# Kernel tuning notes

Measured on AMD Instinct MI355X. Metric: run time of the kernel, lower is better.

The kernel has to match this reference:

```python
import jax, jax.numpy as jnp
import numpy as np

N = 50000
E = 800000
G = 64  # number of graphs in each batch
IN_DIM = 128
HID = 64
NEG_SLOPE = 0.2


def _glorot(key, shape):
    fan = shape[0] + shape[-1] if len(shape) == 2 else int(np.prod(shape[1:])) + shape[-1]
    lim = float(np.sqrt(6.0 / fan))
    return jax.random.uniform(key, shape, jnp.float32, -lim, lim)


def setup_inputs() -> dict:
    key = jax.random.key(0)
    ks = jax.random.split(key, 16)
    x1 = jax.random.normal(ks[0], (N, IN_DIM), jnp.float32)
    x2 = jax.random.normal(ks[1], (N, IN_DIM), jnp.float32)
    edge_index1 = jax.random.randint(ks[2], (2, E), 0, N, jnp.int64)
    edge_index2 = jax.random.randint(ks[3], (2, E), 0, N, jnp.int64)
    batch1 = jnp.sort(jax.random.randint(ks[4], (N,), 0, G, jnp.int64))
    batch2 = jnp.sort(jax.random.randint(ks[5], (N,), 0, G, jnp.int64))
    # conv1: GATConv(IN_DIM, HID, heads=4)
    W1 = _glorot(ks[6], (IN_DIM, 4 * HID))
    a_src1 = _glorot(ks[7], (1, 4, HID))
    a_dst1 = _glorot(ks[8], (1, 4, HID))
    b1 = jnp.zeros((4 * HID,), jnp.float32)
    # conv2: GATConv(4*HID, HID, heads=1)
    W2 = _glorot(ks[9], (4 * HID, HID))
    a_src2 = _glorot(ks[10], (1, 1, HID))
    a_dst2 = _glorot(ks[11], (1, 1, HID))
    b2 = jnp.zeros((HID,), jnp.float32)
    return {"x1": x1, "edge_index1": edge_index1, "batch1": batch1,
            "x2": x2, "edge_index2": edge_index2, "batch2": batch2,
            "W1": W1, "a_src1": a_src1, "a_dst1": a_dst1, "b1": b1,
            "W2": W2, "a_src2": a_src2, "a_dst2": a_dst2, "b2": b2}


def gat_conv(x, src, dst, W, a_src, a_dst, b, n_nodes, heads, out_dim):
    """PyG GATConv with add_self_loops=True, negative_slope=0.2, concat=True."""
    h = (x @ W).reshape(n_nodes, heads, out_dim)            # [N,H,D]
    alpha_s = jnp.sum(h * a_src, axis=-1)                   # [N,H]
    alpha_d = jnp.sum(h * a_dst, axis=-1)                   # [N,H]
    e = alpha_s[src] + alpha_d[dst]                         # [E',H]
    e = jax.nn.leaky_relu(e, NEG_SLOPE)
    # segment softmax over incoming edges of each destination node
    e_max = jax.ops.segment_max(e, dst, num_segments=n_nodes)
    ex = jnp.exp(e - e_max[dst])
    denom = jax.ops.segment_sum(ex, dst, num_segments=n_nodes)
    alpha = ex / (denom[dst] + 1e-16)                       # [E',H]
    msg = h[src] * alpha[:, :, None]                        # [E',H,D]
    out = jax.ops.segment_sum(msg, dst, num_segments=n_nodes)
    return out.reshape(n_nodes, heads * out_dim) + b


def embed(x, edge_index, batch, W1, a_src1, a_dst1, b1, W2, a_src2, a_dst2, b2):
    loops = jnp.arange(N, dtype=edge_index.dtype)
    src = jnp.concatenate([edge_index[0], loops])
    dst = jnp.concatenate([edge_index[1], loops])
    h = jax.nn.elu(gat_conv(x, src, dst, W1, a_src1, a_dst1, b1, N, 4, HID))
    h = jax.nn.elu(gat_conv(h, src, dst, W2, a_src2, a_dst2, b2, N, 1, HID))
    # global_mean_pool over graph ids
    sums = jax.ops.segment_sum(h, batch, num_segments=G)
    cnt = jax.ops.segment_sum(jnp.ones((N,), h.dtype), batch, num_segments=G)
    return sums / jnp.maximum(cnt, 1.0)[:, None]


def reference(x1, edge_index1, batch1, x2, edge_index2, batch2,
              W1, a_src1, a_dst1, b1, W2, a_src2, a_dst2, b2):
    emb1 = embed(x1, edge_index1, batch1, W1, a_src1, a_dst1, b1, W2, a_src2, a_dst2, b2)
    emb2 = embed(x2, edge_index2, batch2, W1, a_src1, a_dst1, b1, W2, a_src2, a_dst2, b2)
    return (emb1, emb2)
```

## Files before the change

kernel.cpp:

```cpp
#include <hip/hip_runtime.h>
#include <cstdint>
#include <cstddef>

#define NNODES 50000
#define NEDGES 800000
#define NGR    64
#define INDIM  128
#define HIDD   64

typedef __attribute__((ext_vector_type(8))) short bf16x8;
typedef __attribute__((ext_vector_type(4))) float f32x4;

__device__ __forceinline__ float lrelu(float x) { return x > 0.f ? x : 0.2f * x; }
__device__ __forceinline__ float eluf(float x)  { return x > 0.f ? x : expm1f(x); }
__device__ __forceinline__ float bf2f(unsigned short u) {
    return __uint_as_float((unsigned int)u << 16);
}
__device__ __forceinline__ unsigned short f2bf(float x) {
    unsigned int u = __float_as_uint(x);
    return (unsigned short)((u + 0x7fffu + ((u >> 16) & 1u)) >> 16);
}

__global__ void cvt_f2b(const float* __restrict__ in, unsigned short* __restrict__ out, int n4) {
    int i = blockIdx.x * 256 + threadIdx.x;
    if (i < n4) {
        float4 v = ((const float4*)in)[i];
        ushort4 o;
        o.x = f2bf(v.x); o.y = f2bf(v.y); o.z = f2bf(v.z); o.w = f2bf(v.w);
        ((ushort4*)out)[i] = o;
    }
}

__global__ void count_dst(const int* __restrict__ ei0, const int* __restrict__ ei1,
                          int* __restrict__ cnt, int E, int N) {
    const int* ei = blockIdx.y ? ei1 : ei0;
    int* c = cnt + blockIdx.y * N;
    int e = blockIdx.x * 256 + threadIdx.x;
    if (e < E) atomicAdd(&c[ei[E + e]], 1);
}

__global__ __launch_bounds__(256) void scan_part(const int* __restrict__ cnt,
                                                 int* __restrict__ psum, int n) {
    __shared__ int ws[4];
    const int* c = cnt + blockIdx.y * n;
    int* p = psum + blockIdx.y * 256;
    int lane = threadIdx.x & 63, w = threadIdx.x >> 6;
    int i = blockIdx.x * 256 + threadIdx.x;
    int v = (i < n) ? c[i] : 0;
    #pragma unroll
    for (int off = 32; off >= 1; off >>= 1) v += __shfl_xor(v, off, 64);
    if (lane == 0) ws[w] = v;
    __syncthreads();
    if (threadIdx.x == 0) p[blockIdx.x] = ws[0] + ws[1] + ws[2] + ws[3];
}

__global__ __launch_bounds__(256) void scan_tops(int* __restrict__ psum,
                                                 int* __restrict__ rp, int nb, int n) {
    __shared__ int wsum[4];
    int* p = psum + blockIdx.x * 256;
    int* r = rp + blockIdx.x * (n + 1);
    int tid = threadIdx.x, lane = tid & 63, w = tid >> 6;
    int v = (tid < nb) ? p[tid] : 0;
    int x = v;
    #pragma unroll
    for (int off = 1; off < 64; off <<= 1) {
        int t = __shfl_up(x, off, 64);
        if (lane >= off) x += t;
    }
    if (lane == 63) wsum[w] = x;
    __syncthreads();
    int add = 0;
    for (int k = 0; k < w; k++) add += wsum[k];
    int incl = x + add;
    if (tid < nb) p[tid] = incl - v;
    if (tid == nb - 1) r[n] = incl;
}

__global__ __launch_bounds__(256) void scan_fin(const int* __restrict__ cnt,
                                                const int* __restrict__ psum,
                                                int* __restrict__ rp, int n) {
    __shared__ int wsum[4];
    const int* c = cnt + blockIdx.y * n;
    const int* p = psum + blockIdx.y * 256;
    int* r = rp + blockIdx.y * (n + 1);
    int tid = threadIdx.x, lane = tid & 63, w = tid >> 6;
    int i = blockIdx.x * 256 + tid;
    int v = (i < n) ? c[i] : 0;
    int x = v;
    #pragma unroll
    for (int off = 1; off < 64; off <<= 1) {
        int t = __shfl_up(x, off, 64);
        if (lane >= off) x += t;
    }
    if (lane == 63) wsum[w] = x;
    __syncthreads();
    int add = p[blockIdx.x];
    for (int k = 0; k < w; k++) add += wsum[k];
    if (i < n) r[i] = x + add - v;
}

__global__ void fill_csr(const int* __restrict__ ei0, const int* __restrict__ ei1,
                         const int* __restrict__ rp, int* __restrict__ fc,
                         int* __restrict__ col, int E, int N) {
    int g = blockIdx.y;
    const int* ei = g ? ei1 : ei0;
    const int* r = rp + g * (N + 1);
    int* f = fc + g * N;
    int* cl = col + (size_t)g * E;
    int e = blockIdx.x * 256 + threadIdx.x;
    if (e < E) {
        int s = ei[e];
        int d = ei[E + e];
        int pos = atomicAdd(&f[d], 1);
        cl[r[d] + pos] = s;
    }
}

template<int BN, int WM, int WN, bool AF32>
__global__ __launch_bounds__(256) void gemm_mfma(const void* __restrict__ A0,
                                                 const void* __restrict__ A1,
                                                 size_t Ags,
                                                 const unsigned short* __restrict__ Bw,
                                                 unsigned short* __restrict__ C,
                                                 size_t Cgs,
                                                 int M, int K, int N,
                                                 const float* __restrict__ a_src,
                                                 const float* __restrict__ a_dst,
                                                 float* __restrict__ as_o,
                                                 float* __restrict__ ad_o,
                                                 int hstride, int ags) {
    constexpr int BM = 128, BK = 64;
    constexpr int MI = WM / 16, NI = WN / 16;
    constexpr int LDA = BK + 8;
    __shared__ unsigned short Asm[BM * LDA];
    __shared__ unsigned short Bsm[BN * LDA];
    int gph = blockIdx.z;
    const float* Af = (const float*)(gph ? A1 : A0);
    const unsigned short* Ab = (const unsigned short*)A0 + (size_t)gph * Ags;
    unsigned short* Cg = C + (size_t)gph * Cgs;
    float* aso = as_o + (size_t)gph * ags;
    float* ado = ad_o + (size_t)gph * ags;
    int tid = threadIdx.x;
    int lane = tid & 63, wave = tid >> 6;
    int l15 = lane & 15, quad = lane >> 4;
    int wm0, wn0;
    if (BN == 128) { wm0 = (wave >> 1) * 64; wn0 = (wave & 1) * 64; }
    else           { wm0 = wave * 32;        wn0 = 0; }
    int row0 = blockIdx.x * BM;
    int c0 = blockIdx.y * BN;

    f32x4 acc[MI][NI];
    #pragma unroll
    for (int mi = 0; mi < MI; mi++)
        #pragma unroll
        for (int ni = 0; ni < NI; ni++)
            acc[mi][ni] = (f32x4){0.f, 0.f, 0.f, 0.f};

    for (int k0 = 0; k0 < K; k0 += BK) {
        #pragma unroll
        for (int q = 0; q < BM / 32; q++) {
            int idx = q * 256 + tid;
            int r = idx >> 3, kc = idx & 7;
            int row = row0 + r;
            if (AF32) {
                float4 v0 = make_float4(0.f, 0.f, 0.f, 0.f), v1 = v0;
                if (row < M) {
                    v0 = *(const float4*)(Af + (size_t)row * K + k0 + kc * 8);
                    v1 = *(const float4*)(Af + (size_t)row * K + k0 + kc * 8 + 4);
                }
                unsigned short t[8] = {f2bf(v0.x), f2bf(v0.y), f2bf(v0.z), f2bf(v0.w),
                                       f2bf(v1.x), f2bf(v1.y), f2bf(v1.z), f2bf(v1.w)};
                *(uint4*)&Asm[r * LDA + kc * 8] = *(uint4*)t;
            } else {
                uint4 v = make_uint4(0u, 0u, 0u, 0u);
                if (row < M) v = *(const uint4*)(Ab + (size_t)row * K + k0 + kc * 8);
                *(uint4*)&Asm[r * LDA + kc * 8] = v;
            }
        }
        #pragma unroll
        for (int q = 0; q < BN / 32; q++) {
            int idx = q * 256 + tid;
            int n  = idx & (BN - 1);
            int kc = idx / BN;
            unsigned short tmp[8];
            #pragma unroll
            for (int j = 0; j < 8; j++)
                tmp[j] = Bw[(size_t)(k0 + kc * 8 + j) * N + c0 + n];
            *(uint4*)&Bsm[n * LDA + kc * 8] = *(uint4*)tmp;
        }
        __syncthreads();
        #pragma unroll
        for (int kb = 0; kb < 2; kb++) {
            bf16x8 af[MI], bfr[NI];
            #pragma unroll
            for (int mi = 0; mi < MI; mi++)
                af[mi] = *(bf16x8*)&Asm[(wm0 + mi * 16 + l15) * LDA + kb * 32 + quad * 8];
            #pragma unroll
            for (int ni = 0; ni < NI; ni++)
                bfr[ni] = *(bf16x8*)&Bsm[(wn0 + ni * 16 + l15) * LDA + kb * 32 + quad * 8];
            #pragma unroll
            for (int mi = 0; mi < MI; mi++)
                #pragma unroll
                for (int ni = 0; ni < NI; ni++)
                    acc[mi][ni] = __builtin_amdgcn_mfma_f32_16x16x32_bf16(
                        af[mi], bfr[ni], acc[mi][ni], 0, 0, 0);
        }
        __syncthreads();
    }
    #pragma unroll
    for (int mi = 0; mi < MI; mi++) {
        #pragma unroll
        for (int r = 0; r < 4; r++) {
            int row = row0 + wm0 + mi * 16 + quad * 4 + r;
            if (row < M) {
                #pragma unroll
                for (int ni = 0; ni < NI; ni++) {
                    int colg = c0 + wn0 + ni * 16 + l15;
                    Cg[(size_t)row * N + colg] = f2bf(acc[mi][ni][r]);
                }
            }
        }
    }
    int headc = (c0 + wn0) >> 6;
    float a_s[NI], a_d[NI];
    #pragma unroll
    for (int ni = 0; ni < NI; ni++) {
        a_s[ni] = a_src[headc * 64 + ni * 16 + l15];
        a_d[ni] = a_dst[headc * 64 + ni * 16 + l15];
    }
    #pragma unroll
    for (int mi = 0; mi < MI; mi++) {
        #pragma unroll
        for (int r = 0; r < 4; r++) {
            float ps = 0.f, pd = 0.f;
            #pragma unroll
            for (int ni = 0; ni < NI; ni++) {
                ps += acc[mi][ni][r] * a_s[ni];
                pd += acc[mi][ni][r] * a_d[ni];
            }
            #pragma unroll
            for (int off = 1; off < 16; off <<= 1) {
                ps += __shfl_xor(ps, off, 64);
                pd += __shfl_xor(pd, off, 64);
            }
            int row = row0 + wm0 + mi * 16 + quad * 4 + r;
            if (l15 == 0 && row < M) {
                aso[row * hstride + headc] = ps;
                ado[row * hstride + headc] = pd;
            }
        }
    }
}

__global__ __launch_bounds__(256) void wcomp4(const int* __restrict__ rp,
                                              const int* __restrict__ col,
                                              const float* __restrict__ as1,
                                              const float* __restrict__ ad1,
                                              float4* __restrict__ w4,
                                              int n, int E, int ags) {
    int g = blockIdx.y;
    const int* r = rp + g * (n + 1);
    const int* cl = col + (size_t)g * E;
    const float4* as4 = (const float4*)(as1 + (size_t)g * ags);
    const float4* ad4 = (const float4*)(ad1 + (size_t)g * ags);
    float4* wg = w4 + (size_t)g * E;
    int node = blockIdx.x * 16 + (threadIdx.x >> 4);
    int l16 = threadIdx.x & 15;
    if (node >= n) return;
    int beg = r[node], end = r[node + 1];
    float4 b = ad4[node];
    for (int j = beg + l16; j < end; j += 16) {
        float4 a = as4[cl[j]];
        float4 w;
        w.x = __expf(lrelu(a.x + b.x)); w.y = __expf(lrelu(a.y + b.y));
        w.z = __expf(lrelu(a.z + b.z)); w.w = __expf(lrelu(a.w + b.w));
        wg[j] = w;
    }
}

__global__ __launch_bounds__(256) void wcomp1(const int* __restrict__ rp,
                                              const int* __restrict__ col,
                                              const float* __restrict__ as2,
                                              const float* __restrict__ ad2,
                                              float* __restrict__ w1,
                                              int n, int E) {
    int g = blockIdx.y;
    const int* r = rp + g * (n + 1);
    const int* cl = col + (size_t)g * E;
    const float* as = as2 + (size_t)g * n;
    const float* ad = ad2 + (size_t)g * n;
    float* wg = w1 + (size_t)g * E;
    int node = blockIdx.x * 16 + (threadIdx.x >> 4);
    int l16 = threadIdx.x & 15;
    if (node >= n) return;
    int beg = r[node], end = r[node + 1];
    float b = ad[node];
    for (int j = beg + l16; j < end; j += 16)
        wg[j] = __expf(lrelu(as[cl[j]] + b));
}

__global__ __launch_bounds__(256) void agg_h4(const unsigned short* __restrict__ h,
                                              size_t hgs,
                                              const float* __restrict__ as_,
                                              const float* __restrict__ ad_, int ags,
                                              const float* __restrict__ w4,
                                              const int* __restrict__ rp,
                                              const int* __restrict__ col,
                                              const float* __restrict__ bias,
                                              unsigned short* __restrict__ out,
                                              size_t ogs, int n, int E) {
    int gph = blockIdx.y;
    const uint2* h2v = (const uint2*)(h + (size_t)gph * hgs);
    const float* as = as_ + (size_t)gph * ags;
    const float* adp = ad_ + (size_t)gph * ags;
    const float* wv = w4 + (size_t)gph * E * 4;
    const int* r = rp + gph * (n + 1);
    const int* cl = col + (size_t)gph * E;
    unsigned short* og = out + (size_t)gph * ogs;

    int wave = threadIdx.x >> 6, lane = threadIdx.x & 63;
    int node = blockIdx.x * 4 + wave;
    if (node >= n) return;
    int head = lane >> 4;
    float w0 = __expf(lrelu(as[node * 4 + head] + adp[node * 4 + head]));
    uint2 hu = h2v[(size_t)node * 64 + lane];
    float den = w0;
    float ax = __uint_as_float(hu.x << 16) * w0;
    float ay = __uint_as_float(hu.x & 0xffff0000u) * w0;
    float az = __uint_as_float(hu.y << 16) * w0;
    float aw = __uint_as_float(hu.y & 0xffff0000u) * w0;
    int beg = __builtin_amdgcn_readfirstlane(r[node]);
    int end = __builtin_amdgcn_readfirstlane(r[node + 1]);
    int j = beg;
    for (; j + 2 <= end; j += 2) {
        int s0 = __builtin_amdgcn_readfirstlane(cl[j]);
        int s1 = __builtin_amdgcn_readfirstlane(cl[j + 1]);
        float wa = wv[j * 4 + head];
        float wb = wv[(j + 1) * 4 + head];
        uint2 u0 = h2v[(size_t)s0 * 64 + lane];
        uint2 u1 = h2v[(size_t)s1 * 64 + lane];
        den += wa + wb;
        ax += __uint_as_float(u0.x << 16) * wa + __uint_as_float(u1.x << 16) * wb;
        ay += __uint_as_float(u0.x & 0xffff0000u) * wa + __uint_as_float(u1.x & 0xffff0000u) * wb;
        az += __uint_as_float(u0.y << 16) * wa + __uint_as_float(u1.y << 16) * wb;
        aw += __uint_as_float(u0.y & 0xffff0000u) * wa + __uint_as_float(u1.y & 0xffff0000u) * wb;
    }
    if (j < end) {
        int s = __builtin_amdgcn_readfirstlane(cl[j]);
        float w = wv[j * 4 + head];
        uint2 u = h2v[(size_t)s * 64 + lane];
        den += w;
        ax += __uint_as_float(u.x << 16) * w;
        ay += __uint_as_float(u.x & 0xffff0000u) * w;
        az += __uint_as_float(u.y << 16) * w;
        aw += __uint_as_float(u.y & 0xffff0000u) * w;
    }
    float rden = 1.f / (den + 1e-16f);
    float4 bv = ((const float4*)bias)[lane];
    ushort4 o;
    o.x = f2bf(eluf(ax * rden + bv.x));
    o.y = f2bf(eluf(ay * rden + bv.y));
    o.z = f2bf(eluf(az * rden + bv.z));
    o.w = f2bf(eluf(aw * rden + bv.w));
    ((ushort4*)og)[(size_t)node * 64 + lane] = o;
}

__global__ __launch_bounds__(256) void agg_h1(const unsigned short* __restrict__ h,
                                              size_t hgs,
                                              const float* __restrict__ as_,
                                              const float* __restrict__ ad_,
                                              const float* __restrict__ w1,
                                              const int* __restrict__ rp,
                                              const int* __restrict__ col,
                                              const float* __restrict__ bias,
                                              float* __restrict__ out,
                                              size_t ogs, int n, int E) {
    int gph = blockIdx.y;
    const unsigned short* hg = h + (size_t)gph * hgs;
    const float* as = as_ + (size_t)gph * n;
    const float* adp = ad_ + (size_t)gph * n;
    const float* wv = w1 + (size_t)gph * E;
    const int* r = rp + gph * (n + 1);
    const int* cl = col + (size_t)gph * E;
    float* og = out + (size_t)gph * ogs;

    int wave = threadIdx.x >> 6, lane = threadIdx.x & 63;
    int node = blockIdx.x * 4 + wave;
    if (node >= n) return;
    float w0 = __expf(lrelu(as[node] + adp[node]));
    float den = w0;
    float acc = w0 * bf2f(hg[(size_t)node * 64 + lane]);
    int beg = __builtin_amdgcn_readfirstlane(r[node]);
    int end = __builtin_amdgcn_readfirstlane(r[node + 1]);
    int j = beg;
    for (; j + 2 <= end; j += 2) {
        int s0 = __builtin_amdgcn_readfirstlane(cl[j]);
        int s1 = __builtin_amdgcn_readfirstlane(cl[j + 1]);
        float wa = wv[j], wb = wv[j + 1];
        float va = bf2f(hg[(size_t)s0 * 64 + lane]);
        float vb = bf2f(hg[(size_t)s1 * 64 + lane]);
        den += wa + wb;
        acc += va * wa + vb * wb;
    }
    if (j < end) {
        int s = __builtin_amdgcn_readfirstlane(cl[j]);
        float w = wv[j];
        den += w;
        acc += w * bf2f(hg[(size_t)s * 64 + lane]);
    }
    float rden = 1.f / (den + 1e-16f);
    og[(size_t)node * 64 + lane] = eluf(acc * rden + bias[lane]);
}

__device__ __forceinline__ int lbound(const int* __restrict__ a, int n, int key) {
    int lo = 0, hi = n;
    while (lo < hi) {
        int mid = (lo + hi) >> 1;
        if (a[mid] < key) lo = mid + 1; else hi = mid;
    }
    return lo;
}

__global__ __launch_bounds__(256) void pool_mean(const float* __restrict__ g2,
                                                 size_t ggs,
                                                 const int* __restrict__ b0,
                                                 const int* __restrict__ b1,
                                                 float* __restrict__ out, int n) {
    __shared__ float red[4][64];
    __shared__ int bnds[2];
    int gph = blockIdx.y;
    const int* batch = gph ? b1 : b0;
    const float* gg = g2 + (size_t)gph * ggs;
    float* og = out + (size_t)gph * NGR * HIDD;
    int g = blockIdx.x;
    if (threadIdx.x < 2) bnds[threadIdx.x] = lbound(batch, n, g + (int)threadIdx.x);
    __syncthreads();
    int s = bnds[0], e = bnds[1];
    int lane = threadIdx.x & 63, wave = threadIdx.x >> 6;
    float acc = 0.f;
    for (int i = s + wave; i < e; i += 4)
        acc += gg[(size_t)i * 64 + lane];
    red[wave][lane] = acc;
    __syncthreads();
    if (wave == 0) {
        float sum = red[0][lane] + red[1][lane] + red[2][lane] + red[3][lane];
        og[g * 64 + lane] = sum / fmaxf((float)(e - s), 1.0f);
    }
}

extern "C" void kernel_launch(void* const* d_in, const int* in_sizes, int n_in,
                              void* d_out, int out_size, void* d_ws, size_t ws_size,
                              hipStream_t stream) {
    const int N = NNODES, E = NEDGES;

    const float* x1 = (const float*)d_in[0];
    const float* x2 = (const float*)d_in[3];
    const int* ei1v = (const int*)d_in[1];
    const int* ei2v = (const int*)d_in[4];
    const int* ba1  = (const int*)d_in[2];
    const int* ba2  = (const int*)d_in[5];
    const float* W1     = (const float*)d_in[6];
    const float* a_src1 = (const float*)d_in[7];
    const float* a_dst1 = (const float*)d_in[8];
    const float* b1     = (const float*)d_in[9];
    const float* W2     = (const float*)d_in[10];
    const float* a_src2 = (const float*)d_in[11];
    const float* a_dst2 = (const float*)d_in[12];
    const float* b2     = (const float*)d_in[13];

    char* ws = (char*)d_ws;
    size_t off = 0;
    auto carve = [&](size_t bytes) -> char* {
        char* p = ws + off;
        off = (off + bytes + 255) & ~(size_t)255;
        return p;
    };
    char* R1 = carve((size_t)2 * N * 256 * 2);
    char* R2 = carve((size_t)2 * N * 256 * 2);
    char* R3 = carve((size_t)2 * E * 16);
    int*   col  = (int*)carve((size_t)2 * E * 4);
    int*   rp   = (int*)carve((size_t)2 * (N + 1) * 4);
    int*   cntN = (int*)carve((size_t)2 * N * 4);
    int*   psum = (int*)carve(2 * 256 * 4);
    float* as1  = (float*)carve((size_t)2 * N * 4 * 4);
    float* ad1  = (float*)carve((size_t)2 * N * 4 * 4);
    float* as2  = (float*)carve((size_t)2 * N * 4);
    float* ad2  = (float*)carve((size_t)2 * N * 4);
    unsigned short* W1b = (unsigned short*)carve(INDIM * 256 * 2);
    unsigned short* W2b = (unsigned short*)carve(256 * HIDD * 2);

    unsigned short* h1 = (unsigned short*)R1;
    unsigned short* g1 = (unsigned short*)R2;
    float4* w4 = (float4*)R3;
    unsigned short* h2 = (unsigned short*)R3;
    float* w2 = (float*)(R3 + (size_t)2 * N * 64 * 2);
    float* g2 = (float*)R1;

    float* outF = (float*)d_out;

    const int nodeBlocks = (N + 3) / 4;
    const int node16Blocks = (N + 15) / 16;
    const int nb = (N + 255) / 256;
    const int eb = (E + 255) / 256;

    cvt_f2b<<<(INDIM * 256 / 4 + 255) / 256, 256, 0, stream>>>(W1, W1b, INDIM * 256 / 4);
    cvt_f2b<<<(256 * HIDD / 4 + 255) / 256, 256, 0, stream>>>(W2, W2b, 256 * HIDD / 4);

    hipMemsetAsync(cntN, 0, (size_t)2 * N * 4, stream);
    count_dst<<<dim3(eb, 2), 256, 0, stream>>>(ei1v, ei2v, cntN, E, N);
    scan_part<<<dim3(nb, 2), 256, 0, stream>>>(cntN, psum, N);
    scan_tops<<<2, 256, 0, stream>>>(psum, rp, nb, N);
    scan_fin<<<dim3(nb, 2), 256, 0, stream>>>(cntN, psum, rp, N);
    hipMemsetAsync(cntN, 0, (size_t)2 * N * 4, stream);
    fill_csr<<<dim3(eb, 2), 256, 0, stream>>>(ei1v, ei2v, rp, cntN, col, E, N);

    gemm_mfma<128, 64, 64, true><<<dim3(391, 2, 2), 256, 0, stream>>>(
        x1, x2, 0, W1b, h1, (size_t)N * 256, N, INDIM, 256,
        a_src1, a_dst1, as1, ad1, 4, N * 4);
    wcomp4<<<dim3(node16Blocks, 2), 256, 0, stream>>>(rp, col, as1, ad1, w4, N, E, N * 4);
    agg_h4<<<dim3(nodeBlocks, 2), 256, 0, stream>>>(h1, (size_t)N * 256, as1, ad1, N * 4,
                                                    (const float*)w4, rp, col, b1,
                                                    g1, (size_t)N * 256, N, E);

    gemm_mfma<64, 32, 64, false><<<dim3(391, 1, 2), 256, 0, stream>>>(
        g1, nullptr, (size_t)N * 256, W2b, h2, (size_t)N * 64, N, 256, HIDD,
        a_src2, a_dst2, as2, ad2, 1, N);
    wcomp1<<<dim3(node16Blocks, 2), 256, 0, stream>>>(rp, col, as2, ad2, w2, N, E);
    agg_h1<<<dim3(nodeBlocks, 2), 256, 0, stream>>>(h2, (size_t)N * 64, as2, ad2, w2,
                                                    rp, col, b2, g2, (size_t)N * 64, N, E);

    pool_mean<<<dim3(NGR, 2), 256, 0, stream>>>(g2, (size_t)N * 64, ba1, ba2, outF, N);
}
```

Before: 586.5 us.

## Fuse edge-weight computation into aggregation kernels via wave shuffles

Removes the separate wcomp4/wcomp1 kernels that precomputed per-edge exp(leaky_relu) weights into a global buffer. The aggregation kernels now load chunks of up to 16 or 64 neighbor indices cooperatively per wave, compute the attention weights in-lane, and broadcast weights and source ids with shuffles. This drops two launches and the write and reread of per-edge weight arrays, at the cost of shuffle overhead and some redundant lanes inside the aggregation loop.

```diff
diff --git a/kernel.cpp b/kernel.cpp
--- a/kernel.cpp
+++ b/kernel.cpp
@@ -252,58 +252,10 @@
     }
 }
 
-__global__ __launch_bounds__(256) void wcomp4(const int* __restrict__ rp,
-                                              const int* __restrict__ col,
-                                              const float* __restrict__ as1,
-                                              const float* __restrict__ ad1,
-                                              float4* __restrict__ w4,
-                                              int n, int E, int ags) {
-    int g = blockIdx.y;
-    const int* r = rp + g * (n + 1);
-    const int* cl = col + (size_t)g * E;
-    const float4* as4 = (const float4*)(as1 + (size_t)g * ags);
-    const float4* ad4 = (const float4*)(ad1 + (size_t)g * ags);
-    float4* wg = w4 + (size_t)g * E;
-    int node = blockIdx.x * 16 + (threadIdx.x >> 4);
-    int l16 = threadIdx.x & 15;
-    if (node >= n) return;
-    int beg = r[node], end = r[node + 1];
-    float4 b = ad4[node];
-    for (int j = beg + l16; j < end; j += 16) {
-        float4 a = as4[cl[j]];
-        float4 w;
-        w.x = __expf(lrelu(a.x + b.x)); w.y = __expf(lrelu(a.y + b.y));
-        w.z = __expf(lrelu(a.z + b.z)); w.w = __expf(lrelu(a.w + b.w));
-        wg[j] = w;
-    }
-}
-
-__global__ __launch_bounds__(256) void wcomp1(const int* __restrict__ rp,
-                                              const int* __restrict__ col,
-                                              const float* __restrict__ as2,
-                                              const float* __restrict__ ad2,
-                                              float* __restrict__ w1,
-                                              int n, int E) {
-    int g = blockIdx.y;
-    const int* r = rp + g * (n + 1);
-    const int* cl = col + (size_t)g * E;
-    const float* as = as2 + (size_t)g * n;
-    const float* ad = ad2 + (size_t)g * n;
-    float* wg = w1 + (size_t)g * E;
-    int node = blockIdx.x * 16 + (threadIdx.x >> 4);
-    int l16 = threadIdx.x & 15;
-    if (node >= n) return;
-    int beg = r[node], end = r[node + 1];
-    float b = ad[node];
-    for (int j = beg + l16; j < end; j += 16)
-        wg[j] = __expf(lrelu(as[cl[j]] + b));
-}
-
 __global__ __launch_bounds__(256) void agg_h4(const unsigned short* __restrict__ h,
                                               size_t hgs,
                                               const float* __restrict__ as_,
                                               const float* __restrict__ ad_, int ags,
-                                              const float* __restrict__ w4,
                                               const int* __restrict__ rp,
                                               const int* __restrict__ col,
                                               const float* __restrict__ bias,
@@ -313,7 +265,6 @@
     const uint2* h2v = (const uint2*)(h + (size_t)gph * hgs);
     const float* as = as_ + (size_t)gph * ags;
     const float* adp = ad_ + (size_t)gph * ags;
-    const float* wv = w4 + (size_t)gph * E * 4;
     const int* r = rp + gph * (n + 1);
     const int* cl = col + (size_t)gph * E;
     unsigned short* og = out + (size_t)gph * ogs;
@@ -321,8 +272,9 @@
     int wave = threadIdx.x >> 6, lane = threadIdx.x & 63;
     int node = blockIdx.x * 4 + wave;
     if (node >= n) return;
-    int head = lane >> 4;
-    float w0 = __expf(lrelu(as[node * 4 + head] + adp[node * 4 + head]));
+    int head = lane >> 4, l15 = lane & 15, q16 = lane & 48;
+    float adv = adp[node * 4 + head];
+    float w0 = __expf(lrelu(as[node * 4 + head] + adv));
     uint2 hu = h2v[(size_t)node * 64 + lane];
     float den = w0;
     float ax = __uint_as_float(hu.x << 16) * w0;
@@ -331,29 +283,35 @@
     float aw = __uint_as_float(hu.y & 0xffff0000u) * w0;
     int beg = __builtin_amdgcn_readfirstlane(r[node]);
     int end = __builtin_amdgcn_readfirstlane(r[node + 1]);
-    int j = beg;
-    for (; j + 2 <= end; j += 2) {
-        int s0 = __builtin_amdgcn_readfirstlane(cl[j]);
-        int s1 = __builtin_amdgcn_readfirstlane(cl[j + 1]);
-        float wa = wv[j * 4 + head];
-        float wb = wv[(j + 1) * 4 + head];
-        uint2 u0 = h2v[(size_t)s0 * 64 + lane];
-        uint2 u1 = h2v[(size_t)s1 * 64 + lane];
-        den += wa + wb;
-        ax += __uint_as_float(u0.x << 16) * wa + __uint_as_float(u1.x << 16) * wb;
-        ay += __uint_as_float(u0.x & 0xffff0000u) * wa + __uint_as_float(u1.x & 0xffff0000u) * wb;
-        az += __uint_as_float(u0.y << 16) * wa + __uint_as_float(u1.y << 16) * wb;
-        aw += __uint_as_float(u0.y & 0xffff0000u) * wa + __uint_as_float(u1.y & 0xffff0000u) * wb;
-    }
-    if (j < end) {
-        int s = __builtin_amdgcn_readfirstlane(cl[j]);
-        float w = wv[j * 4 + head];
-        uint2 u = h2v[(size_t)s * 64 + lane];
-        den += w;
-        ax += __uint_as_float(u.x << 16) * w;
-        ay += __uint_as_float(u.x & 0xffff0000u) * w;
-        az += __uint_as_float(u.y << 16) * w;
-        aw += __uint_as_float(u.y & 0xffff0000u) * w;
+    for (int j = beg; j < end; j += 16) {
+        int m = end - j; if (m > 16) m = 16;
+        int colv = cl[j + (l15 < m ? l15 : m - 1)];
+        float av = as[colv * 4 + head];
+        float w = __expf(lrelu(av + adv));
+        int e = 0;
+        for (; e + 2 <= m; e += 2) {
+            float wa = __shfl(w, q16 | e);
+            float wb = __shfl(w, q16 | (e + 1));
+            int s0 = __shfl(colv, e);
+            int s1 = __shfl(colv, e + 1);
+            uint2 u0 = h2v[(size_t)s0 * 64 + lane];
+            uint2 u1 = h2v[(size_t)s1 * 64 + lane];
+            den += wa + wb;
+            ax += __uint_as_float(u0.x << 16) * wa + __uint_as_float(u1.x << 16) * wb;
+            ay += __uint_as_float(u0.x & 0xffff0000u) * wa + __uint_as_float(u1.x & 0xffff0000u) * wb;
+            az += __uint_as_float(u0.y << 16) * wa + __uint_as_float(u1.y << 16) * wb;
+            aw += __uint_as_float(u0.y & 0xffff0000u) * wa + __uint_as_float(u1.y & 0xffff0000u) * wb;
+        }
+        if (e < m) {
+            float wa = __shfl(w, q16 | e);
+            int s0 = __shfl(colv, e);
+            uint2 u0 = h2v[(size_t)s0 * 64 + lane];
+            den += wa;
+            ax += __uint_as_float(u0.x << 16) * wa;
+            ay += __uint_as_float(u0.x & 0xffff0000u) * wa;
+            az += __uint_as_float(u0.y << 16) * wa;
+            aw += __uint_as_float(u0.y & 0xffff0000u) * wa;
+        }
     }
     float rden = 1.f / (den + 1e-16f);
     float4 bv = ((const float4*)bias)[lane];
@@ -369,7 +327,6 @@
                                               size_t hgs,
                                               const float* __restrict__ as_,
                                               const float* __restrict__ ad_,
-                                              const float* __restrict__ w1,
                                               const int* __restrict__ rp,
                                               const int* __restrict__ col,
                                               const float* __restrict__ bias,
@@ -379,7 +336,6 @@
     const unsigned short* hg = h + (size_t)gph * hgs;
     const float* as = as_ + (size_t)gph * n;
     const float* adp = ad_ + (size_t)gph * n;
-    const float* wv = w1 + (size_t)gph * E;
     const int* r = rp + gph * (n + 1);
     const int* cl = col + (size_t)gph * E;
     float* og = out + (size_t)gph * ogs;
@@ -387,26 +343,33 @@
     int wave = threadIdx.x >> 6, lane = threadIdx.x & 63;
     int node = blockIdx.x * 4 + wave;
     if (node >= n) return;
-    float w0 = __expf(lrelu(as[node] + adp[node]));
+    float adv = adp[node];
+    float w0 = __expf(lrelu(as[node] + adv));
     float den = w0;
     float acc = w0 * bf2f(hg[(size_t)node * 64 + lane]);
     int beg = __builtin_amdgcn_readfirstlane(r[node]);
     int end = __builtin_amdgcn_readfirstlane(r[node + 1]);
-    int j = beg;
-    for (; j + 2 <= end; j += 2) {
-        int s0 = __builtin_amdgcn_readfirstlane(cl[j]);
-        int s1 = __builtin_amdgcn_readfirstlane(cl[j + 1]);
-        float wa = wv[j], wb = wv[j + 1];
-        float va = bf2f(hg[(size_t)s0 * 64 + lane]);
-        float vb = bf2f(hg[(size_t)s1 * 64 + lane]);
-        den += wa + wb;
-        acc += va * wa + vb * wb;
-    }
-    if (j < end) {
-        int s = __builtin_amdgcn_readfirstlane(cl[j]);
-        float w = wv[j];
-        den += w;
-        acc += w * bf2f(hg[(size_t)s * 64 + lane]);
+    for (int j = beg; j < end; j += 64) {
+        int m = end - j; if (m > 64) m = 64;
+        int colv = cl[j + (lane < m ? lane : m - 1)];
+        float w = __expf(lrelu(as[colv] + adv));
+        int e = 0;
+        for (; e + 2 <= m; e += 2) {
+            float wa = __shfl(w, e);
+            float wb = __shfl(w, e + 1);
+            int s0 = __shfl(colv, e);
+            int s1 = __shfl(colv, e + 1);
+            float va = bf2f(hg[(size_t)s0 * 64 + lane]);
+            float vb = bf2f(hg[(size_t)s1 * 64 + lane]);
+            den += wa + wb;
+            acc += va * wa + vb * wb;
+        }
+        if (e < m) {
+            float wa = __shfl(w, e);
+            int s0 = __shfl(colv, e);
+            den += wa;
+            acc += wa * bf2f(hg[(size_t)s0 * 64 + lane]);
+        }
     }
     float rden = 1.f / (den + 1e-16f);
     og[(size_t)node * 64 + lane] = eluf(acc * rden + bias[lane]);
@@ -477,7 +440,7 @@
     };
     char* R1 = carve((size_t)2 * N * 256 * 2);
     char* R2 = carve((size_t)2 * N * 256 * 2);
-    char* R3 = carve((size_t)2 * E * 16);
+    char* R3 = carve((size_t)2 * N * 64 * 2);
     int*   col  = (int*)carve((size_t)2 * E * 4);
     int*   rp   = (int*)carve((size_t)2 * (N + 1) * 4);
     int*   cntN = (int*)carve((size_t)2 * N * 4);
@@ -491,15 +454,12 @@
 
     unsigned short* h1 = (unsigned short*)R1;
     unsigned short* g1 = (unsigned short*)R2;
-    float4* w4 = (float4*)R3;
     unsigned short* h2 = (unsigned short*)R3;
-    float* w2 = (float*)(R3 + (size_t)2 * N * 64 * 2);
     float* g2 = (float*)R1;
 
     float* outF = (float*)d_out;
 
     const int nodeBlocks = (N + 3) / 4;
-    const int node16Blocks = (N + 15) / 16;
     const int nb = (N + 255) / 256;
     const int eb = (E + 255) / 256;
 
@@ -517,16 +477,13 @@
     gemm_mfma<128, 64, 64, true><<<dim3(391, 2, 2), 256, 0, stream>>>(
         x1, x2, 0, W1b, h1, (size_t)N * 256, N, INDIM, 256,
         a_src1, a_dst1, as1, ad1, 4, N * 4);
-    wcomp4<<<dim3(node16Blocks, 2), 256, 0, stream>>>(rp, col, as1, ad1, w4, N, E, N * 4);
     agg_h4<<<dim3(nodeBlocks, 2), 256, 0, stream>>>(h1, (size_t)N * 256, as1, ad1, N * 4,
-                                                    (const float*)w4, rp, col, b1,
-                                                    g1, (size_t)N * 256, N, E);
+                                                    rp, col, b1, g1, (size_t)N * 256, N, E);
 
     gemm_mfma<64, 32, 64, false><<<dim3(391, 1, 2), 256, 0, stream>>>(
         g1, nullptr, (size_t)N * 256, W2b, h2, (size_t)N * 64, N, 256, HIDD,
         a_src2, a_dst2, as2, ad2, 1, N);
-    wcomp1<<<dim3(node16Blocks, 2), 256, 0, stream>>>(rp, col, as2, ad2, w2, N, E);
-    agg_h1<<<dim3(nodeBlocks, 2), 256, 0, stream>>>(h2, (size_t)N * 64, as2, ad2, w2,
+    agg_h1<<<dim3(nodeBlocks, 2), 256, 0, stream>>>(h2, (size_t)N * 64, as2, ad2,
                                                     rp, col, b2, g2, (size_t)N * 64, N, E);
 
     pool_mean<<<dim3(NGR, 2), 256, 0, stream>>>(g2, (size_t)N * 64, ba1, ba2, outF, N);
```

Result: faster. 572.9 us (-2.3%).
